# Optimization experiments

Measured on AMD Instinct MI355X. Metric: run time of the kernel, lower is better.

Reference implementation:

```python
import jax, jax.numpy as jnp
import numpy as np

CH = 512
HEADS = 4
GROUPS = 32  # _groups(512) -> 32
EPS = 1e-5


def setup_inputs() -> dict:
    key = jax.random.key(0)
    ks = jax.random.split(key, 7)
    b, c, h, w = 16, CH, 32, 32
    sd = 1.0 / np.sqrt(c)
    return {
        "x": jax.random.normal(ks[0], (b, c, h, w), dtype=jnp.float32),
        "gamma": jnp.ones((c,), jnp.float32),
        "beta": jnp.zeros((c,), jnp.float32),
        "w_qkv": jax.random.normal(ks[1], (3 * c, c), dtype=jnp.float32) * sd,
        "b_qkv": jax.random.normal(ks[2], (3 * c,), dtype=jnp.float32) * 0.01,
        "w_proj": jax.random.normal(ks[3], (c, c), dtype=jnp.float32) * sd,
        "b_proj": jax.random.normal(ks[4], (c,), dtype=jnp.float32) * 0.01,
    }


def _group_norm(x, gamma, beta):
    b, c, h, w = x.shape
    xg = x.reshape(b, GROUPS, -1)  # (b, G, c//G * h * w)
    mu = jnp.mean(xg, axis=-1, keepdims=True)
    var = jnp.var(xg, axis=-1, keepdims=True)
    xn = ((xg - mu) * jax.lax.rsqrt(var + EPS)).reshape(b, c, h, w)
    return xn * gamma[None, :, None, None] + beta[None, :, None, None]


def reference(x, gamma, beta, w_qkv, b_qkv, w_proj, b_proj):
    b, c, h, w = x.shape
    hd = c // HEADS
    xn = _group_norm(x, gamma, beta)
    # 1x1 conv == channel matmul
    qkv = jnp.einsum('oc,bchw->bohw', w_qkv, xn) + b_qkv[None, :, None, None]
    qkv = qkv.reshape(b, 3, HEADS, hd, h * w)
    q, k, v = qkv[:, 0], qkv[:, 1], qkv[:, 2]  # (b, H, hd, n)
    scale = hd ** -0.5
    attn = jax.nn.softmax(jnp.einsum('bhcn,bhcm->bhnm', q * scale, k), axis=-1)
    out = jnp.einsum('bhnm,bhcm->bhcn', attn, v).reshape(b, c, h, w)
    out = jnp.einsum('oc,bchw->bohw', w_proj, out) + b_proj[None, :, None, None]
    return x + out
```

## Files before the change

kernel.cpp:

```cpp
#include <hip/hip_runtime.h>

#define CH 512
#define HEADS 4
#define HD 128
#define NPIX 1024
#define BATCH 16
#define GROUPS 32
#define GSZ 16
#define EPS 1e-5f

typedef _Float16 f16;
typedef _Float16 f16x8 __attribute__((ext_vector_type(8)));
typedef _Float16 f16x4 __attribute__((ext_vector_type(4)));
typedef float f32x4 __attribute__((ext_vector_type(4)));
typedef float f32x16 __attribute__((ext_vector_type(16)));

__device__ __forceinline__ void gld16(const f16* g, f16* l) {
    __builtin_amdgcn_global_load_lds((__attribute__((address_space(1))) const void*)g,
                                     (__attribute__((address_space(3))) void*)l, 16, 0, 0);
}

__global__ __launch_bounds__(256, 2) void k_pre(const float* __restrict__ x, const float* __restrict__ gamma,
                                                const float* __restrict__ beta, f16* __restrict__ xnT,
                                                const float* __restrict__ wq, const float* __restrict__ wp,
                                                f16* __restrict__ wqT, f16* __restrict__ wpT) {
    __shared__ float xs[GSZ * NPIX];
    __shared__ float red[8];
    __shared__ float stat2[2];
    int bidx = blockIdx.x;
    if (bidx >= 512) {
        int c = (bidx - 512) * 256 + threadIdx.x;
        {
            int ot = c >> 13, kbl = (c >> 7) & 63, ol = c & 127;
            const float* s = wq + ((size_t)(ot * 128 + ol)) * CH + kbl * 8;
            f32x4 a = *(const f32x4*)s, b2 = *(const f32x4*)(s + 4);
            f16x8 v;
            v[0] = (f16)a.x; v[1] = (f16)a.y; v[2] = (f16)a.z; v[3] = (f16)a.w;
            v[4] = (f16)b2.x; v[5] = (f16)b2.y; v[6] = (f16)b2.z; v[7] = (f16)b2.w;
            *(f16x8*)(wqT + (size_t)c * 8) = v;
        }
        if (c < 32768) {
            int ot = c >> 13, kbl = (c >> 7) & 63, ol = c & 127;
            const float* s = wp + ((size_t)(ot * 128 + ol)) * CH + kbl * 8;
            f32x4 a = *(const f32x4*)s, b2 = *(const f32x4*)(s + 4);
            f16x8 v;
            v[0] = (f16)a.x; v[1] = (f16)a.y; v[2] = (f16)a.z; v[3] = (f16)a.w;
            v[4] = (f16)b2.x; v[5] = (f16)b2.y; v[6] = (f16)b2.z; v[7] = (f16)b2.w;
            *(f16x8*)(wpT + (size_t)c * 8) = v;
        }
        return;
    }
    int g = bidx & 31, b = bidx >> 5;
    const f32x4* x4 = (const f32x4*)(x + ((size_t)(b * GROUPS + g)) * (GSZ * NPIX));
    float s = 0.f, ss = 0.f;
    for (int i = threadIdx.x; i < GSZ * NPIX / 4; i += 256) {
        f32x4 v = x4[i];
        *(f32x4*)&xs[i * 4] = v;
        s  += v.x + v.y + v.z + v.w;
        ss += v.x * v.x + v.y * v.y + v.z * v.z + v.w * v.w;
    }
    for (int off = 32; off; off >>= 1) { s += __shfl_down(s, off); ss += __shfl_down(ss, off); }
    int wv = threadIdx.x >> 6, ln = threadIdx.x & 63;
    if (ln == 0) { red[wv] = s; red[4 + wv] = ss; }
    __syncthreads();
    if (threadIdx.x == 0) {
        float S = red[0] + red[1] + red[2] + red[3];
        float SS = red[4] + red[5] + red[6] + red[7];
        float mu = S / (GSZ * NPIX);
        float var = SS / (GSZ * NPIX) - mu * mu;
        stat2[0] = mu; stat2[1] = rsqrtf(var + EPS);
    }
    __syncthreads();
    float mu = stat2[0], rstd = stat2[1];
    int ch = threadIdx.x >> 7;
    int n  = threadIdx.x & 127;
    float gl[8], bl[8];
#pragma unroll
    for (int i = 0; i < 8; i++) {
        float gv = gamma[g * 16 + ch * 8 + i] * rstd;
        gl[i] = gv;
        bl[i] = beta[g * 16 + ch * 8 + i] - mu * gv;
    }
    f16* tb0 = xnT + ((size_t)(b * 8)) * 65536 + (g * 2 + ch) * 1024 + n * 8;
#pragma unroll
    for (int nt = 0; nt < 8; nt++) {
        f16x8 o;
#pragma unroll
        for (int i = 0; i < 8; i++)
            o[i] = (f16)(xs[(ch * 8 + i) * 1024 + nt * 128 + n] * gl[i] + bl[i]);
        *(f16x8*)(tb0 + (size_t)nt * 65536) = o;
    }
}

__global__ __launch_bounds__(256, 3) void k_qkv(const f16* __restrict__ wT, const float* __restrict__ bias,
                                                const f16* __restrict__ xnT, f16* __restrict__ qF,
                                                f16* __restrict__ kTl, f16* __restrict__ vTl) {
    int nt = blockIdx.x, ot = blockIdx.y, b = blockIdx.z;
    int o0 = ot * 128;
    __shared__ union SM {
        struct { f16 As[8192]; f16 Bs[8192]; } s;
        f16 Cf[16384];
    } sm;
    __shared__ float biasS[128];
    if (threadIdx.x < 128) biasS[threadIdx.x] = bias[o0 + threadIdx.x];
    int tid = threadIdx.x, lane = tid & 63, wv = tid >> 6;
    int wr = wv >> 1, wc = wv & 1;
    int l15 = lane & 15, quad = lane >> 4;
    const f16* wA = wT + (size_t)ot * 65536;
    const f16* xB = xnT + ((size_t)(b * 8 + nt)) * 65536;
    f32x4 acc[4][4] = {};
    for (int kk = 0; kk < CH; kk += 64) {
        __syncthreads();
        const f16* sa = wA + (size_t)(kk >> 3) * 1024;
        const f16* sb = xB + (size_t)(kk >> 3) * 1024;
#pragma unroll
        for (int i = 0; i < 4; i++) {
            int s = wv * 4 + i;
            gld16(sa + (size_t)(s * 64 + lane) * 8, sm.s.As + s * 512);
            gld16(sb + (size_t)(s * 64 + lane) * 8, sm.s.Bs + s * 512);
        }
        __syncthreads();
#pragma unroll
        for (int dk = 0; dk < 2; dk++) {
            f16x8 af[4], bf[4];
#pragma unroll
            for (int t = 0; t < 4; t++) {
                af[t] = *(const f16x8*)(sm.s.As + (dk * 4 + quad) * 1024 + (wr * 64 + t * 16 + l15) * 8);
                bf[t] = *(const f16x8*)(sm.s.Bs + (dk * 4 + quad) * 1024 + (wc * 64 + t * 16 + l15) * 8);
            }
#pragma unroll
            for (int tm = 0; tm < 4; tm++)
#pragma unroll
                for (int tn = 0; tn < 4; tn++)
                    acc[tm][tn] = __builtin_amdgcn_mfma_f32_16x16x32_f16(af[tm], bf[tn], acc[tm][tn], 0, 0, 0);
        }
    }
    __syncthreads();
    int which = ot >> 2, h = ot & 3;
#pragma unroll
    for (int tm = 0; tm < 4; tm++)
#pragma unroll
        for (int tn = 0; tn < 4; tn++) {
            int ob = wr * 64 + tm * 16 + quad * 4;
            int n  = wc * 64 + tn * 16 + l15;
            f16x4 pv;
#pragma unroll
            for (int r = 0; r < 4; r++) pv[r] = (f16)(acc[tm][tn][r] + biasS[ob + r]);
            if (which == 0) {
                int addr = ((((n >> 5) * 2 + ((n >> 4) & 1)) * 4 + (ob >> 5)) * 512)
                         + ((ob >> 3) & 3) * 128 + (n & 15) * 8 + (quad & 1) * 4;
                *(f16x4*)&sm.Cf[addr] = pv;
            } else if (which == 1) {
                int addr = (ob >> 3) * 1024 + n * 8 + (quad & 1) * 4;
                *(f16x4*)&sm.Cf[addr] = pv;
            } else {
#pragma unroll
                for (int r = 0; r < 4; r++)
                    sm.Cf[(n >> 3) * 1024 + (ob + r) * 8 + (n & 7)] = pv[r];
            }
        }
    __syncthreads();
    f16* tb = (which == 0) ? (qF + ((size_t)((b * 4 + h) * 8 + nt)) * 16384)
            : (which == 1) ? (kTl + ((size_t)((b * 4 + h) * 8 + nt)) * 16384)
                           : (vTl + ((size_t)((b * 4 + h) * 8 + nt)) * 16384);
#pragma unroll
    for (int i = 0; i < 8; i++) {
        int cid = tid + i * 256;
        *(f16x8*)(tb + (size_t)cid * 8) = *(const f16x8*)(sm.Cf + cid * 8);
    }
}

__global__ __launch_bounds__(256, 2) void k_attn(const f16* __restrict__ qF, const f16* __restrict__ kTl,
                                                 const f16* __restrict__ vTl, f16* __restrict__ oT) {
    extern __shared__ f16 smem[];
    int bid = blockIdx.x;
    int nt = bid >> 6, group = bid & 63;
    int b = group >> 2, h = group & 3;
    int tid = threadIdx.x, lane = tid & 63, wv = tid >> 6;
    int l31 = lane & 31, halfl = lane >> 5;
    const f16* qb = qF + ((size_t)(group * 8 + nt)) * 16384;
    const f16* kb = kTl + (size_t)group * 8 * 16384;
    const f16* vb = vTl + (size_t)group * 8 * 16384;
    f16* Pw = smem + 32768 + wv * 2048;

    f16x8 aq[8];
    {
        int bq = (wv * 2 + ((lane >> 4) & 1)) * 4;
#pragma unroll
        for (int s = 0; s < 8; s++) {
            f16x8 v = *(const f16x8*)(qb + (bq + (s >> 1)) * 512 + ((s & 1) * 2 + halfl) * 128 + (lane & 15) * 8);
            aq[s] = v * (f16)(0.08838834764831845f * 1.4426950408889634f);
        }
    }

    float m_i = -1e30f, l_i = 0.f;
    f32x16 oacc[4] = {};

    auto stage = [&](int mc, f16* dst) {
        if (wv < 2) {
            const f16* src = kb + (size_t)(mc >> 1) * 16384 + (size_t)(mc & 1) * 512;
#pragma unroll
            for (int i = 0; i < 8; i++)
                gld16(src + (size_t)(wv * 8 + i) * 1024 + lane * 8, dst + (wv * 8 + i) * 512);
        } else {
            const f16* src = vb + (size_t)mc * 8192;
#pragma unroll
            for (int i = 0; i < 8; i++)
                gld16(src + (size_t)((wv - 2) * 8 + i) * 512 + lane * 8, dst + 8192 + ((wv - 2) * 8 + i) * 512);
        }
    };

    stage(0, smem);

    for (int mc = 0; mc < 16; mc++) {
        __syncthreads();
        f16* Kc = smem + (mc & 1) * 16384;
        f16* Vc = Kc + 8192;
        if (mc < 15) stage(mc + 1, smem + ((mc + 1) & 1) * 16384);

        f32x16 st0 = {}, st1 = {};
#pragma unroll
        for (int s = 0; s < 8; s++) {
            f16x8 k0 = *(const f16x8*)&Kc[(s * 2 + halfl) * 512 + l31 * 8];
            f16x8 k1 = *(const f16x8*)&Kc[(s * 2 + halfl) * 512 + (32 + l31) * 8];
            st0 = __builtin_amdgcn_mfma_f32_32x32x16_f16(k0, aq[s], st0, 0, 0, 0);
            st1 = __builtin_amdgcn_mfma_f32_32x32x16_f16(k1, aq[s], st1, 0, 0, 0);
        }

        float a[16];
#pragma unroll
        for (int i = 0; i < 16; i++) a[i] = fmaxf(st0[i], st1[i]);
#pragma unroll
        for (int i = 0; i < 8; i++) a[i] = fmaxf(a[i], a[i + 8]);
#pragma unroll
        for (int i = 0; i < 4; i++) a[i] = fmaxf(a[i], a[i + 4]);
        float mx = fmaxf(fmaxf(a[0], a[1]), fmaxf(a[2], a[3]));
        mx = fmaxf(mx, __shfl_xor(mx, 32));

        bool full = !__all(mx <= m_i + 8.f);
        float mnew = m_i, alpha = 1.f;
        if (full) {
            mnew = fmaxf(m_i, mx);
            alpha = __builtin_amdgcn_exp2f(m_i - mnew);
            m_i = mnew;
        }

        float r[16];
#pragma unroll
        for (int i = 0; i < 16; i++) {
            float p0 = __builtin_amdgcn_exp2f(st0[i] - mnew);
            float p1 = __builtin_amdgcn_exp2f(st1[i] - mnew);
            st0[i] = p0; st1[i] = p1;
            r[i] = p0 + p1;
        }
#pragma unroll
        for (int i = 0; i < 8; i++) r[i] += r[i + 8];
#pragma unroll
        for (int i = 0; i < 4; i++) r[i] += r[i + 4];
        float rs = (r[0] + r[1]) + (r[2] + r[3]);
        rs += __shfl_xor(rs, 32);
        if (full) {
            l_i = l_i * alpha + rs;
#pragma unroll
            for (int dt = 0; dt < 4; dt++)
#pragma unroll
                for (int i = 0; i < 16; i++) oacc[dt][i] *= alpha;
        } else {
            l_i += rs;
        }

#pragma unroll
        for (int g = 0; g < 4; g++) {
            f16x4 pv0, pv1;
#pragma unroll
            for (int rr = 0; rr < 4; rr++) { pv0[rr] = (f16)st0[g * 4 + rr]; pv1[rr] = (f16)st1[g * 4 + rr]; }
            *(f16x4*)&Pw[l31 * 64 + ((g ^ (l31 & 7)) << 3) + (halfl << 2)] = pv0;
            *(f16x4*)&Pw[l31 * 64 + (((4 + g) ^ (l31 & 7)) << 3) + (halfl << 2)] = pv1;
        }

#pragma unroll
        for (int ks = 0; ks < 4; ks++) {
            f16x8 pf = *(const f16x8*)&Pw[l31 * 64 + (((ks * 2 + halfl) ^ (l31 & 7)) << 3)];
#pragma unroll
            for (int dt = 0; dt < 4; dt++) {
                f16x8 vf = *(const f16x8*)&Vc[(ks * 2 + halfl) * 1024 + (dt * 32 + l31) * 8];
                oacc[dt] = __builtin_amdgcn_mfma_f32_32x32x16_f16(vf, pf, oacc[dt], 0, 0, 0);
            }
        }
    }

    __syncthreads();
    {
        float inv = 1.f / l_i;
        int n = wv * 32 + l31;
#pragma unroll
        for (int dt = 0; dt < 4; dt++)
#pragma unroll
            for (int g = 0; g < 4; g++) {
                f16x4 ov;
#pragma unroll
                for (int rr = 0; rr < 4; rr++) ov[rr] = (f16)(oacc[dt][g * 4 + rr] * inv);
                int cbl = dt * 4 + g;
                *(f16x4*)&smem[n * 128 + ((cbl ^ (n & 15)) << 3) + (halfl << 2)] = ov;
            }
    }
    __syncthreads();
    f16* ob = oT + ((size_t)(b * 8 + nt)) * 65536;
#pragma unroll
    for (int i = 0; i < 8; i++) {
        int cid = tid + i * 256;
        int cbl = cid >> 7, n = cid & 127;
        f16x8 v = *(const f16x8*)&smem[n * 128 + ((cbl ^ (n & 15)) << 3)];
        *(f16x8*)(ob + (size_t)(h * 16 + cbl) * 1024 + n * 8) = v;
    }
}

__global__ __launch_bounds__(256, 3) void k_proj(const f16* __restrict__ wT, const float* __restrict__ bias,
                                                 const f16* __restrict__ oT, const float* __restrict__ x,
                                                 float* __restrict__ out) {
    int nt = blockIdx.x, ot = blockIdx.y, b = blockIdx.z;
    int n0 = nt * 128, o0 = ot * 128;
    __shared__ union SM {
        struct { f16 As[8192]; f16 Bs[8192]; } s;
        f16 Cs[128][136];
    } sm;
    __shared__ float biasS[128];
    if (threadIdx.x < 128) biasS[threadIdx.x] = bias[o0 + threadIdx.x];
    int tid = threadIdx.x, lane = tid & 63, wv = tid >> 6;
    int wr = wv >> 1, wc = wv & 1;
    int l15 = lane & 15, quad = lane >> 4;
    const f16* wA = wT + (size_t)ot * 65536;
    const f16* xB = oT + ((size_t)(b * 8 + nt)) * 65536;
    f32x4 acc[4][4] = {};
    for (int kk = 0; kk < CH; kk += 64) {
        __syncthreads();
        const f16* sa = wA + (size_t)(kk >> 3) * 1024;
        const f16* sb = xB + (size_t)(kk >> 3) * 1024;
#pragma unroll
        for (int i = 0; i < 4; i++) {
            int s = wv * 4 + i;
            gld16(sa + (size_t)(s * 64 + lane) * 8, sm.s.As + s * 512);
            gld16(sb + (size_t)(s * 64 + lane) * 8, sm.s.Bs + s * 512);
        }
        __syncthreads();
#pragma unroll
        for (int dk = 0; dk < 2; dk++) {
            f16x8 af[4], bf[4];
#pragma unroll
            for (int t = 0; t < 4; t++) {
                af[t] = *(const f16x8*)(sm.s.As + (dk * 4 + quad) * 1024 + (wr * 64 + t * 16 + l15) * 8);
                bf[t] = *(const f16x8*)(sm.s.Bs + (dk * 4 + quad) * 1024 + (wc * 64 + t * 16 + l15) * 8);
            }
#pragma unroll
            for (int tm = 0; tm < 4; tm++)
#pragma unroll
                for (int tn = 0; tn < 4; tn++)
                    acc[tm][tn] = __builtin_amdgcn_mfma_f32_16x16x32_f16(af[tm], bf[tn], acc[tm][tn], 0, 0, 0);
        }
    }
    __syncthreads();
#pragma unroll
    for (int tm = 0; tm < 4; tm++)
#pragma unroll
        for (int tn = 0; tn < 4; tn++)
#pragma unroll
            for (int r = 0; r < 4; r++) {
                int o = wr * 64 + tm * 16 + quad * 4 + r;
                int n = wc * 64 + tn * 16 + l15;
                sm.Cs[o][n] = (f16)(acc[tm][tn][r] + biasS[o]);
            }
    __syncthreads();
#pragma unroll
    for (int i = 0; i < 8; i++) {
        int cid = tid + i * 256;
        int row = cid >> 4, off = (cid & 15) * 8;
        f16x8 v = *(const f16x8*)&sm.Cs[row][off];
        size_t gofs = ((size_t)(b * CH) + o0 + row) * NPIX + n0 + off;
        const float* xp = x + gofs;
        float* op = out + gofs;
        f32x4 o0v, o1v;
        o0v.x = xp[0] + (float)v[0]; o0v.y = xp[1] + (float)v[1];
        o0v.z = xp[2] + (float)v[2]; o0v.w = xp[3] + (float)v[3];
        o1v.x = xp[4] + (float)v[4]; o1v.y = xp[5] + (float)v[5];
        o1v.z = xp[6] + (float)v[6]; o1v.w = xp[7] + (float)v[7];
        *(f32x4*)op = o0v; *(f32x4*)(op + 4) = o1v;
    }
}

extern "C" void kernel_launch(void* const* d_in, const int* in_sizes, int n_in,
                              void* d_out, int out_size, void* d_ws, size_t ws_size,
                              hipStream_t stream) {
    const float* x     = (const float*)d_in[0];
    const float* gamma = (const float*)d_in[1];
    const float* beta  = (const float*)d_in[2];
    const float* wqkv  = (const float*)d_in[3];
    const float* bqkv  = (const float*)d_in[4];
    const float* wproj = (const float*)d_in[5];
    const float* bproj = (const float*)d_in[6];
    float* out = (float*)d_out;

    char* p = (char*)d_ws;
    f16* wqT = (f16*)p;           p += (size_t)3 * CH * CH * 2;
    f16* wpT = (f16*)p;           p += (size_t)CH * CH * 2;
    f16* xnT = (f16*)p;           p += (size_t)BATCH * NPIX * CH * 2;
    f16* qF  = (f16*)p;           p += (size_t)BATCH * HEADS * NPIX * HD * 2;
    f16* kTl = (f16*)p;           p += (size_t)BATCH * HEADS * NPIX * HD * 2;
    f16* vTl = (f16*)p;           p += (size_t)BATCH * HEADS * NPIX * HD * 2;
    f16* oT  = (f16*)p;           p += (size_t)BATCH * NPIX * CH * 2;

    k_pre<<<dim3(896), 256, 0, stream>>>(x, gamma, beta, xnT, wqkv, wproj, wqT, wpT);
    k_qkv<<<dim3(8, 12, BATCH), 256, 0, stream>>>(wqT, bqkv, xnT, qF, kTl, vTl);

    hipFuncSetAttribute((const void*)k_attn, hipFuncAttributeMaxDynamicSharedMemorySize, 81920);
    k_attn<<<dim3(512), 256, 81920, stream>>>(qF, kTl, vTl, oT);

    k_proj<<<dim3(8, 4, BATCH), 256, 0, stream>>>(wpT, bproj, oT, x, out);
}
```

Baseline: 201.2 us.

## Rework QKV GEMM into double-buffered 256x128 tiles with 32x32 MFMA

The QKV projection kernel now uses 512-thread blocks that each compute a 256-row by 128-pixel output tile, covering two heads, so the grid halves. The K loop moves to 32-wide steps with a two-stage LDS double buffer, explicit waitcnt and barrier scheduling, and 32x32x16 MFMA instead of 16x16x32. This aims to overlap global loads with compute and raise reuse of the activation tile per block. In exchange it uses more LDS, fewer blocks, and a hand-written synchronisation scheme that is easy to get wrong.

Result: slower. 210.2 us (+4.5%).

```diff
diff --git a/kernel.cpp b/kernel.cpp
--- a/kernel.cpp
+++ b/kernel.cpp
@@ -92,81 +92,121 @@
     }
 }
 
-__global__ __launch_bounds__(256, 3) void k_qkv(const f16* __restrict__ wT, const float* __restrict__ bias,
+__global__ __launch_bounds__(512, 4) void k_qkv(const f16* __restrict__ wT, const float* __restrict__ bias,
                                                 const f16* __restrict__ xnT, f16* __restrict__ qF,
                                                 f16* __restrict__ kTl, f16* __restrict__ vTl) {
-    int nt = blockIdx.x, ot = blockIdx.y, b = blockIdx.z;
-    int o0 = ot * 128;
-    __shared__ union SM {
-        struct { f16 As[8192]; f16 Bs[8192]; } s;
-        f16 Cf[16384];
-    } sm;
-    __shared__ float biasS[128];
-    if (threadIdx.x < 128) biasS[threadIdx.x] = bias[o0 + threadIdx.x];
+    __shared__ f16 lds[32768];
+    __shared__ float biasS[256];
+    int nt = blockIdx.x, mt = blockIdx.y, b = blockIdx.z;
     int tid = threadIdx.x, lane = tid & 63, wv = tid >> 6;
-    int wr = wv >> 1, wc = wv & 1;
-    int l15 = lane & 15, quad = lane >> 4;
-    const f16* wA = wT + (size_t)ot * 65536;
+    int wm = wv >> 1, wn = wv & 1;
+    int l31 = lane & 31, halfl = lane >> 5;
+    if (tid < 256) biasS[tid] = bias[mt * 256 + tid];
+
+    const f16* wA = wT + (size_t)(mt * 2) * 65536;
     const f16* xB = xnT + ((size_t)(b * 8 + nt)) * 65536;
-    f32x4 acc[4][4] = {};
-    for (int kk = 0; kk < CH; kk += 64) {
-        __syncthreads();
-        const f16* sa = wA + (size_t)(kk >> 3) * 1024;
-        const f16* sb = xB + (size_t)(kk >> 3) * 1024;
-#pragma unroll
-        for (int i = 0; i < 4; i++) {
-            int s = wv * 4 + i;
-            gld16(sa + (size_t)(s * 64 + lane) * 8, sm.s.As + s * 512);
-            gld16(sb + (size_t)(s * 64 + lane) * 8, sm.s.Bs + s * 512);
-        }
-        __syncthreads();
-#pragma unroll
-        for (int dk = 0; dk < 2; dk++) {
-            f16x8 af[4], bf[4];
-#pragma unroll
-            for (int t = 0; t < 4; t++) {
-                af[t] = *(const f16x8*)(sm.s.As + (dk * 4 + quad) * 1024 + (wr * 64 + t * 16 + l15) * 8);
-                bf[t] = *(const f16x8*)(sm.s.Bs + (dk * 4 + quad) * 1024 + (wc * 64 + t * 16 + l15) * 8);
+
+    f32x16 a00 = {}, a01 = {}, a10 = {}, a11 = {};
+
+    auto stage = [&](int kk, int pb) {
+        f16* As = lds + pb * 8192;
+        f16* Bs = lds + 16384 + pb * 4096;
+#pragma unroll
+        for (int i = 0; i < 2; i++) {
+            int u = i * 512 + tid;
+            int kb = u >> 8, r = u & 255;
+            gld16(wA + (size_t)(r >> 7) * 65536 + (kk * 4 + kb) * 1024 + (r & 127) * 8, As + u * 8);
+        }
+        {
+            int kb = tid >> 7, p = tid & 127;
+            gld16(xB + (size_t)(kk * 4 + kb) * 1024 + p * 8, Bs + tid * 8);
+        }
+    };
+
+    auto compute = [&](int pb) {
+        const f16* As = lds + pb * 8192;
+        const f16* Bs = lds + 16384 + pb * 4096;
+#pragma unroll
+        for (int ks = 0; ks < 2; ks++) {
+            int ko = ks * 2 + halfl;
+            f16x8 af0 = *(const f16x8*)&As[ko * 2048 + (wm * 64 + l31) * 8];
+            f16x8 af1 = *(const f16x8*)&As[ko * 2048 + (wm * 64 + 32 + l31) * 8];
+            f16x8 bf0 = *(const f16x8*)&Bs[ko * 1024 + (wn * 64 + l31) * 8];
+            f16x8 bf1 = *(const f16x8*)&Bs[ko * 1024 + (wn * 64 + 32 + l31) * 8];
+            a00 = __builtin_amdgcn_mfma_f32_32x32x16_f16(af0, bf0, a00, 0, 0, 0);
+            a01 = __builtin_amdgcn_mfma_f32_32x32x16_f16(af0, bf1, a01, 0, 0, 0);
+            a10 = __builtin_amdgcn_mfma_f32_32x32x16_f16(af1, bf0, a10, 0, 0, 0);
+            a11 = __builtin_amdgcn_mfma_f32_32x32x16_f16(af1, bf1, a11, 0, 0, 0);
+        }
+    };
+
+    stage(0, 0);
+    stage(1, 1);
+    for (int kk = 0; kk < 15; ++kk) {
+        int pb = kk & 1;
+        asm volatile("s_waitcnt vmcnt(3)" ::: "memory");
+        __builtin_amdgcn_sched_barrier(0);
+        __builtin_amdgcn_s_barrier();
+        __builtin_amdgcn_sched_barrier(0);
+        compute(pb);
+        __builtin_amdgcn_sched_barrier(0);
+        asm volatile("s_waitcnt lgkmcnt(0)" ::: "memory");
+        __builtin_amdgcn_s_barrier();
+        __builtin_amdgcn_sched_barrier(0);
+        if (kk < 14) stage(kk + 2, pb);
+    }
+    asm volatile("s_waitcnt vmcnt(0)" ::: "memory");
+    __builtin_amdgcn_sched_barrier(0);
+    __builtin_amdgcn_s_barrier();
+    __builtin_amdgcn_sched_barrier(0);
+    compute(1);
+    __builtin_amdgcn_sched_barrier(0);
+    asm volatile("s_waitcnt lgkmcnt(0)" ::: "memory");
+    __builtin_amdgcn_s_barrier();
+    __builtin_amdgcn_sched_barrier(0);
+
+    int which = mt >> 1;
+    f16* Cf = lds + ((wm >= 2) ? 16384 : 0);
+    const f32x16* accp[4] = { &a00, &a01, &a10, &a11 };
+#pragma unroll
+    for (int rt = 0; rt < 2; rt++)
+#pragma unroll
+        for (int pt = 0; pt < 2; pt++) {
+            const f32x16& ac = *accp[rt * 2 + pt];
+            int n = wn * 64 + pt * 32 + l31;
+#pragma unroll
+            for (int g2 = 0; g2 < 4; g2++) {
+                int row_full = wv * 64 - (wm >= 2 ? 0 : 0);
+                int ob = (wm & 1) * 64 + rt * 32 + g2 * 8 + halfl * 4;
+                int rfull = wm * 64 + rt * 32 + g2 * 8 + halfl * 4;
+                (void)row_full;
+                f16x4 pv;
+#pragma unroll
+                for (int r = 0; r < 4; r++) pv[r] = (f16)(ac[g2 * 4 + r] + biasS[rfull + r]);
+                if (which == 0) {
+                    int addr = ((((n >> 5) * 2 + ((n >> 4) & 1)) * 4 + (ob >> 5)) * 512)
+                             + ((ob >> 3) & 3) * 128 + (n & 15) * 8 + ((ob >> 2) & 1) * 4;
+                    *(f16x4*)&Cf[addr] = pv;
+                } else if (which == 1) {
+                    int addr = (ob >> 3) * 1024 + n * 8 + ((ob >> 2) & 1) * 4;
+                    *(f16x4*)&Cf[addr] = pv;
+                } else {
+#pragma unroll
+                    for (int r = 0; r < 4; r++)
+                        Cf[(n >> 3) * 1024 + (ob + r) * 8 + (n & 7)] = pv[r];
+                }
             }
-#pragma unroll
-            for (int tm = 0; tm < 4; tm++)
-#pragma unroll
-                for (int tn = 0; tn < 4; tn++)
-                    acc[tm][tn] = __builtin_amdgcn_mfma_f32_16x16x32_f16(af[tm], bf[tn], acc[tm][tn], 0, 0, 0);
-        }
-    }
-    __syncthreads();
-    int which = ot >> 2, h = ot & 3;
-#pragma unroll
-    for (int tm = 0; tm < 4; tm++)
-#pragma unroll
-        for (int tn = 0; tn < 4; tn++) {
-            int ob = wr * 64 + tm * 16 + quad * 4;
-            int n  = wc * 64 + tn * 16 + l15;
-            f16x4 pv;
-#pragma unroll
-            for (int r = 0; r < 4; r++) pv[r] = (f16)(acc[tm][tn][r] + biasS[ob + r]);
-            if (which == 0) {
-                int addr = ((((n >> 5) * 2 + ((n >> 4) & 1)) * 4 + (ob >> 5)) * 512)
-                         + ((ob >> 3) & 3) * 128 + (n & 15) * 8 + (quad & 1) * 4;
-                *(f16x4*)&sm.Cf[addr] = pv;
-            } else if (which == 1) {
-                int addr = (ob >> 3) * 1024 + n * 8 + (quad & 1) * 4;
-                *(f16x4*)&sm.Cf[addr] = pv;
-            } else {
-#pragma unroll
-                for (int r = 0; r < 4; r++)
-                    sm.Cf[(n >> 3) * 1024 + (ob + r) * 8 + (n & 7)] = pv[r];
-            }
-        }
-    __syncthreads();
-    f16* tb = (which == 0) ? (qF + ((size_t)((b * 4 + h) * 8 + nt)) * 16384)
-            : (which == 1) ? (kTl + ((size_t)((b * 4 + h) * 8 + nt)) * 16384)
-                           : (vTl + ((size_t)((b * 4 + h) * 8 + nt)) * 16384);
+        }
+    __syncthreads();
+    int h0 = (mt * 2) & 3;
+    f16* base = (which == 0) ? qF : (which == 1) ? kTl : vTl;
+    f16* tb0 = base + ((size_t)((b * 4 + h0) * 8 + nt)) * 16384;
+    f16* tb1 = base + ((size_t)((b * 4 + h0 + 1) * 8 + nt)) * 16384;
 #pragma unroll
     for (int i = 0; i < 8; i++) {
-        int cid = tid + i * 256;
-        *(f16x8*)(tb + (size_t)cid * 8) = *(const f16x8*)(sm.Cf + cid * 8);
+        int cid = tid + i * 512;
+        f16* dst = ((cid < 2048) ? tb0 : tb1) + (size_t)(cid & 2047) * 8;
+        *(f16x8*)dst = *(const f16x8*)&lds[cid * 8];
     }
 }
 
@@ -409,7 +449,7 @@
     f16* oT  = (f16*)p;           p += (size_t)BATCH * NPIX * CH * 2;
 
     k_pre<<<dim3(896), 256, 0, stream>>>(x, gamma, beta, xnT, wqkv, wproj, wqT, wpT);
-    k_qkv<<<dim3(8, 12, BATCH), 256, 0, stream>>>(wqT, bqkv, xnT, qF, kTl, vTl);
+    k_qkv<<<dim3(8, 6, BATCH), 512, 0, stream>>>(wqT, bqkv, xnT, qF, kTl, vTl);
 
     hipFuncSetAttribute((const void*)k_attn, hipFuncAttributeMaxDynamicSharedMemorySize, 81920);
     k_attn<<<dim3(512), 256, 81920, stream>>>(qF, kTl, vTl, oT);
```
